# Performance work log

Measured on AMD Instinct MI355X. Metric: run time of the kernel, lower is better.

Reference implementation:

```python
import jax, jax.numpy as jnp
import numpy as np

N = 50000
E = 1600000
DIM = 128
RC = 5.0
DEPTH = 3


def setup_inputs() -> dict:
    key = jax.random.key(0)
    kv, ke, ks, kd, kw, kb, krs, ksig = jax.random.split(key, 8)
    v = jax.random.normal(kv, (N, DIM), dtype=jnp.float32)
    # edge distances in [0, rc]
    e = jax.random.uniform(ke, (E, 1), dtype=jnp.float32) * RC
    src = jax.random.randint(ks, (E,), 0, N, dtype=jnp.int32)
    dst = jax.random.randint(kd, (E,), 0, N, dtype=jnp.int32)
    # learned params: A = nn.Linear(dim, dim); rs, sigma = torch.rand(1)
    A_w = jax.random.normal(kw, (DIM, DIM), dtype=jnp.float32) / np.sqrt(DIM)
    A_b = jax.random.normal(kb, (DIM,), dtype=jnp.float32) * 0.01
    rs = jax.random.uniform(krs, (1,), dtype=jnp.float32)
    sigma = jax.random.uniform(ksig, (1,), dtype=jnp.float32)
    return {"v": v, "e": e, "src": src, "dst": dst,
            "A_w": A_w, "A_b": A_b, "rs": rs, "sigma": sigma}


def _edge_envelope(r, rs, sigma):
    # exp(-(r-rs)^2/sigma^2) * 0.5 * cos(pi*r/rc) * (r < rc)
    gauss = jnp.exp(-jnp.square(r - rs) / jnp.square(sigma))
    cutoff = 0.5 * jnp.cos(np.pi * r / RC) * (r < RC).astype(r.dtype)
    return gauss * cutoff


def reference(v, e, src, dst, A_w, A_b, rs, sigma):
    f = _edge_envelope(e, rs, sigma)  # [E, 1]
    cur = v
    for _ in range(DEPTH):
        msg = f * cur[src]  # gather src node feats, weight by edge envelope: [E, DIM]
        svf = jax.ops.segment_sum(msg, dst, num_segments=N)  # scatter-sum to dst: [N, DIM]
        cur = jax.nn.relu((svf + v) @ A_w.T + A_b)  # linear + relu, skip from original v
    return cur
```

## Files before the change

### kernel.cpp

```cpp
#include <hip/hip_runtime.h>
#include <math.h>

#define N_NODES 50000
#define N_PAD   50048
#define N_EDGES 1600000
#define DIM     128
#define RCUT    5.0f
#define NGROUP  (N_PAD / 64)
#define NB_PRE  512
#define CH_PRE  (N_EDGES / NB_PRE)
#define NB_CONV 6250
#define NB_WPREP 8
#define NB_SUB  8
#define B_SUB   (NB_PRE / NB_SUB)
#define XPAD    136

typedef __attribute__((ext_vector_type(8))) __bf16 bf16x8;
typedef __attribute__((ext_vector_type(4))) float  f32x4;

__device__ __forceinline__ float bf_lo(unsigned int u) { return __uint_as_float(u << 16); }
__device__ __forceinline__ float bf_hi(unsigned int u) { return __uint_as_float(u & 0xffff0000u); }
__device__ __forceinline__ unsigned short f2bf(float x) {
    unsigned int u = __float_as_uint(x);
    u += 0x7fffu + ((u >> 16) & 1u);
    return (unsigned short)(u >> 16);
}

__global__ __launch_bounds__(256) void preA_kernel(
        const float* __restrict__ v, unsigned short* __restrict__ vb,
        const float* __restrict__ Aw, uint4* __restrict__ wfrag,
        const int* __restrict__ dst, int* __restrict__ partial) {
    int b = blockIdx.x;
    if (b < NB_CONV) {
        int i = b * 256 + threadIdx.x;
        float4 x = ((const float4*)v)[i];
        uint2 o;
        o.x = (unsigned)f2bf(x.x) | ((unsigned)f2bf(x.y) << 16);
        o.y = (unsigned)f2bf(x.z) | ((unsigned)f2bf(x.w) << 16);
        ((uint2*)vb)[i] = o;
    } else if (b < NB_CONV + NB_WPREP) {
        int t = (b - NB_CONV) * 256 + threadIdx.x;
        int lane = t & 63, nt = (t >> 6) & 7, kk = t >> 9;
        int n  = nt * 16 + (lane & 15);
        int k0 = kk * 32 + (lane >> 4) * 8;
        unsigned short h[8];
        #pragma unroll
        for (int i = 0; i < 8; ++i) h[i] = f2bf(Aw[n * DIM + k0 + i]);
        uint4 o;
        o.x = h[0] | ((unsigned)h[1] << 16); o.y = h[2] | ((unsigned)h[3] << 16);
        o.z = h[4] | ((unsigned)h[5] << 16); o.w = h[6] | ((unsigned)h[7] << 16);
        wfrag[t] = o;
    } else {
        __shared__ int h[NGROUP];
        int cb = b - NB_CONV - NB_WPREP, tid = threadIdx.x;
        for (int g = tid; g < NGROUP; g += 256) h[g] = 0;
        __syncthreads();
        int beg = cb * CH_PRE, end = beg + CH_PRE;
        for (int i = beg + tid; i < end; i += 256)
            atomicAdd(&h[dst[i] >> 6], 1);
        __syncthreads();
        for (int g = tid; g < NGROUP; g += 256) partial[cb * NGROUP + g] = h[g];
    }
}

__global__ __launch_bounds__(256) void ktot2_kernel(const int* __restrict__ partial,
                                                    int* __restrict__ partial2) {
    int gb = blockIdx.x & 3, bb = blockIdx.x >> 2;
    int g = gb * 256 + threadIdx.x;
    if (g >= NGROUP) return;
    int s = 0;
    int b0 = bb * B_SUB;
    for (int b = b0; b < b0 + B_SUB; ++b) s += partial[b * NGROUP + g];
    partial2[bb * NGROUP + g] = s;
}

__global__ __launch_bounds__(256) void kscan_kernel(const int* __restrict__ partial2,
                                                    int* __restrict__ goff) {
    __shared__ int part[256];
    int tid = threadIdx.x;
    int i0 = tid * 4;
    int v[4]; int s = 0;
    #pragma unroll
    for (int k = 0; k < 4; ++k) {
        int i = i0 + k; int t = 0;
        if (i < NGROUP) {
            #pragma unroll
            for (int bb = 0; bb < NB_SUB; ++bb) t += partial2[bb * NGROUP + i];
        }
        v[k] = t; s += t;
    }
    part[tid] = s; __syncthreads();
    for (int d = 1; d < 256; d <<= 1) {
        int val = (tid >= d) ? part[tid - d] : 0;
        __syncthreads(); part[tid] += val; __syncthreads();
    }
    int run = (tid == 0) ? 0 : part[tid - 1];
    #pragma unroll
    for (int k = 0; k < 4; ++k) {
        int i = i0 + k;
        if (i < NGROUP) { goff[i] = run; run += v[k]; }
    }
    if (tid == 0) goff[NGROUP] = N_EDGES;
}

__global__ __launch_bounds__(256) void kbase2_kernel(const int* __restrict__ partial,
                                                     const int* __restrict__ partial2,
                                                     const int* __restrict__ goff,
                                                     int* __restrict__ pbase) {
    int gb = blockIdx.x & 3, bb = blockIdx.x >> 2;
    int g = gb * 256 + threadIdx.x;
    if (g >= NGROUP) return;
    int run = goff[g];
    for (int b2 = 0; b2 < bb; ++b2) run += partial2[b2 * NGROUP + g];
    int b0 = bb * B_SUB;
    for (int b = b0; b < b0 + B_SUB; ++b) {
        pbase[b * NGROUP + g] = run;
        run += partial[b * NGROUP + g];
    }
}

__global__ __launch_bounds__(512) void reorder_kernel(
        const float* __restrict__ e,
        const int*   __restrict__ src,
        const int*   __restrict__ dst,
        const float* __restrict__ rs,
        const float* __restrict__ sigma,
        const int*   __restrict__ pbase,
        int2* __restrict__ metaT) {
    __shared__ int base[NGROUP];
    __shared__ int cnt[NGROUP];
    int b = blockIdx.x, tid = threadIdx.x;
    for (int g = tid; g < NGROUP; g += 512) { base[g] = pbase[b * NGROUP + g]; cnt[g] = 0; }
    __syncthreads();
    float rsv = rs[0], sg = sigma[0];
    int beg = b * CH_PRE, end = beg + CH_PRE;
    for (int i = beg + tid; i < end; i += 512) {
        float r  = e[i];
        float d  = r - rsv;
        float gauss = expf(-(d * d) / (sg * sg));
        float cut   = 0.5f * cosf(r * (float)(M_PI / (double)RCUT));
        cut = (r < RCUT) ? cut : 0.0f;
        float fe = gauss * cut;
        int dn = dst[i];
        int g  = dn >> 6;
        int lr = atomicAdd(&cnt[g], 1);
        metaT[base[g] + lr] = make_int2(src[i] * (DIM * 2) | ((dn & 63) << 24),
                                        __float_as_int(fe));
    }
}

__global__ __launch_bounds__(256) void tagsort_kernel(
        const int2* __restrict__ metaT,
        const int*  __restrict__ goff,
        int2* __restrict__ meta,
        int*  __restrict__ off) {
    __shared__ int cnt[64], base[64], cur[64];
    int g = blockIdx.x, tid = threadIdx.x;
    int sbeg = goff[g], send = goff[g + 1];
    if (tid < 64) cnt[tid] = 0;
    __syncthreads();
    for (int i = sbeg + tid; i < send; i += 256)
        atomicAdd(&cnt[(metaT[i].x >> 24) & 63], 1);
    __syncthreads();
    if (tid == 0) {
        int run = 0;
        #pragma unroll
        for (int t = 0; t < 64; ++t) { base[t] = run; cur[t] = run; run += cnt[t]; }
    }
    __syncthreads();
    if (tid < 64) {
        int node = g * 64 + tid;
        if (node <= N_NODES) off[node] = sbeg + base[tid];
    }
    __syncthreads();
    for (int i = sbeg + tid; i < send; i += 256) {
        int2 m = metaT[i];
        int tag = (m.x >> 24) & 63;
        int lr = atomicAdd(&cur[tag], 1);
        meta[sbeg + lr] = make_int2(m.x & 0x00FFFFFF, m.y);
    }
}

#define EDGE2(mx, mf, rr)                                        \
    do {                                                         \
        float ff = __int_as_float(mf);                           \
        a0 = fmaf(ff, bf_lo(rr), a0);                            \
        a1 = fmaf(ff, bf_hi(rr), a1);                            \
    } while (0)

__global__ __launch_bounds__(512, 6) void layer_kernel(
        const unsigned short* __restrict__ cur,
        const unsigned short* __restrict__ vb,
        const int2*  __restrict__ meta,
        const int*   __restrict__ off,
        const uint4* __restrict__ wfrag,
        const float* __restrict__ bias,
        unsigned short* __restrict__ out_bf,
        float* __restrict__ out_f,
        int last) {
    __shared__ unsigned short xlds[64 * XPAD];
    int tid  = threadIdx.x;
    int wv   = tid >> 6, lane = tid & 63;
    int g    = blockIdx.x;
    int n0   = g * 64 + wv * 8;

    int offidx = n0 + ((lane < 9) ? lane : 8);
    if (offidx > N_NODES) offidx = N_NODES;
    int myoff = off[offidx];

    const char* basec = (const char*)cur + lane * 4;

    #pragma unroll 1
    for (int q = 0; q < 8; ++q) {
        int nl = wv * 8 + q;
        int n  = n0 + q;
        float a0 = 0.f, a1 = 0.f;
        if (n < N_NODES) {
            unsigned vv = *(const unsigned*)((const char*)vb + (size_t)n * (DIM * 2) + lane * 4);
            a0 = bf_lo(vv); a1 = bf_hi(vv);
            int beg = __builtin_amdgcn_readlane(myoff, q);
            int end = __builtin_amdgcn_readlane(myoff, q + 1);
            int c = beg;
            if ((c & 1) && c < end) {
                int2 m = meta[c];
                unsigned rr = *(const unsigned*)(basec + (unsigned)m.x);
                EDGE2(m.x, m.y, rr);
                ++c;
            }
            for (; c + 16 <= end; c += 16) {
                int4 m0 = *(const int4*)(meta + c);
                int4 m1 = *(const int4*)(meta + c + 2);
                int4 m2 = *(const int4*)(meta + c + 4);
                int4 m3 = *(const int4*)(meta + c + 6);
                int4 m4 = *(const int4*)(meta + c + 8);
                int4 m5 = *(const int4*)(meta + c + 10);
                int4 m6 = *(const int4*)(meta + c + 12);
                int4 m7 = *(const int4*)(meta + c + 14);
                unsigned r0  = *(const unsigned*)(basec + (unsigned)m0.x);
                unsigned r1  = *(const unsigned*)(basec + (unsigned)m0.z);
                unsigned r2  = *(const unsigned*)(basec + (unsigned)m1.x);
                unsigned r3  = *(const unsigned*)(basec + (unsigned)m1.z);
                unsigned r4  = *(const unsigned*)(basec + (unsigned)m2.x);
                unsigned r5  = *(const unsigned*)(basec + (unsigned)m2.z);
                unsigned r6  = *(const unsigned*)(basec + (unsigned)m3.x);
                unsigned r7  = *(const unsigned*)(basec + (unsigned)m3.z);
                unsigned r8  = *(const unsigned*)(basec + (unsigned)m4.x);
                unsigned r9  = *(const unsigned*)(basec + (unsigned)m4.z);
                unsigned r10 = *(const unsigned*)(basec + (unsigned)m5.x);
                unsigned r11 = *(const unsigned*)(basec + (unsigned)m5.z);
                unsigned r12 = *(const unsigned*)(basec + (unsigned)m6.x);
                unsigned r13 = *(const unsigned*)(basec + (unsigned)m6.z);
                unsigned r14 = *(const unsigned*)(basec + (unsigned)m7.x);
                unsigned r15 = *(const unsigned*)(basec + (unsigned)m7.z);
                EDGE2(m0.x, m0.y, r0);  EDGE2(m0.z, m0.w, r1);
                EDGE2(m1.x, m1.y, r2);  EDGE2(m1.z, m1.w, r3);
                EDGE2(m2.x, m2.y, r4);  EDGE2(m2.z, m2.w, r5);
                EDGE2(m3.x, m3.y, r6);  EDGE2(m3.z, m3.w, r7);
                EDGE2(m4.x, m4.y, r8);  EDGE2(m4.z, m4.w, r9);
                EDGE2(m5.x, m5.y, r10); EDGE2(m5.z, m5.w, r11);
                EDGE2(m6.x, m6.y, r12); EDGE2(m6.z, m6.w, r13);
                EDGE2(m7.x, m7.y, r14); EDGE2(m7.z, m7.w, r15);
            }
            if (c + 8 <= end) {
                int4 m0 = *(const int4*)(meta + c);
                int4 m1 = *(const int4*)(meta + c + 2);
                int4 m2 = *(const int4*)(meta + c + 4);
                int4 m3 = *(const int4*)(meta + c + 6);
                unsigned r0 = *(const unsigned*)(basec + (unsigned)m0.x);
                unsigned r1 = *(const unsigned*)(basec + (unsigned)m0.z);
                unsigned r2 = *(const unsigned*)(basec + (unsigned)m1.x);
                unsigned r3 = *(const unsigned*)(basec + (unsigned)m1.z);
                unsigned r4 = *(const unsigned*)(basec + (unsigned)m2.x);
                unsigned r5 = *(const unsigned*)(basec + (unsigned)m2.z);
                unsigned r6 = *(const unsigned*)(basec + (unsigned)m3.x);
                unsigned r7 = *(const unsigned*)(basec + (unsigned)m3.z);
                EDGE2(m0.x, m0.y, r0); EDGE2(m0.z, m0.w, r1);
                EDGE2(m1.x, m1.y, r2); EDGE2(m1.z, m1.w, r3);
                EDGE2(m2.x, m2.y, r4); EDGE2(m2.z, m2.w, r5);
                EDGE2(m3.x, m3.y, r6); EDGE2(m3.z, m3.w, r7);
                c += 8;
            }
            for (; c < end; ++c) {
                int2 m = meta[c];
                unsigned rr = *(const unsigned*)(basec + (unsigned)m.x);
                EDGE2(m.x, m.y, rr);
            }
        }
        *(unsigned*)(xlds + nl * XPAD + lane * 2) =
            (unsigned)f2bf(a0) | ((unsigned)f2bf(a1) << 16);
    }
    __syncthreads();

    int quad = lane >> 4, l16 = lane & 15;
    int rb = wv >> 1, nh = wv & 1;
    f32x4 acc[4];
    #pragma unroll
    for (int j = 0; j < 4; ++j) acc[j] = (f32x4){0.f, 0.f, 0.f, 0.f};

    const unsigned short* xp = xlds + (rb * 16 + l16) * XPAD + quad * 8;
    #pragma unroll
    for (int kk = 0; kk < 4; ++kk) {
        bf16x8 af = *(const bf16x8*)(xp + kk * 32);
        #pragma unroll
        for (int j = 0; j < 4; ++j) {
            uint4 w = wfrag[(kk * 8 + nh * 4 + j) * 64 + lane];
            bf16x8 bfr = __builtin_bit_cast(bf16x8, w);
            acc[j] = __builtin_amdgcn_mfma_f32_16x16x32_bf16(af, bfr, acc[j], 0, 0, 0);
        }
    }

    int orow0 = g * 64 + rb * 16 + quad * 4;
    #pragma unroll
    for (int j = 0; j < 4; ++j) {
        int col = (nh * 4 + j) * 16 + l16;
        float b = bias[col];
        #pragma unroll
        for (int r = 0; r < 4; ++r) {
            int orow = orow0 + r;
            if (orow < N_NODES) {
                float val = fmaxf(acc[j][r] + b, 0.f);
                if (last) out_f[(size_t)orow * DIM + col] = val;
                else      out_bf[(size_t)orow * DIM + col] = f2bf(val);
            }
        }
    }
}

extern "C" void kernel_launch(void* const* d_in, const int* in_sizes, int n_in,
                              void* d_out, int out_size, void* d_ws, size_t ws_size,
                              hipStream_t stream) {
    const float* v     = (const float*)d_in[0];
    const float* e     = (const float*)d_in[1];
    const int*   src   = (const int*)  d_in[2];
    const int*   dst   = (const int*)  d_in[3];
    const float* Aw    = (const float*)d_in[4];
    const float* Ab    = (const float*)d_in[5];
    const float* rs    = (const float*)d_in[6];
    const float* sigma = (const float*)d_in[7];
    float* out = (float*)d_out;

    char* p = (char*)d_ws;
    int2*           meta  = (int2*)p;            p += (size_t)N_EDGES * 8;
    unsigned short* bufV  = (unsigned short*)p;  p += (size_t)N_PAD * DIM * 2;
    unsigned short* bufA  = (unsigned short*)p;  p += (size_t)N_PAD * DIM * 2;
    unsigned short* bufB  = (unsigned short*)p;  p += (size_t)N_PAD * DIM * 2;
    uint4*          wfrag = (uint4*)p;           p += 2048 * 16;
    int*            off   = (int*)p;             p += (size_t)(N_NODES + 1) * 4;
    int*            goff  = (int*)p;             p += (NGROUP + 2) * 4;
    int2* metaT    = (int2*)bufA;
    int*  partial  = (int*)bufB;
    int*  pbase    = partial + NB_PRE * NGROUP;
    int*  partial2 = pbase + NB_PRE * NGROUP;

    preA_kernel<<<NB_CONV + NB_WPREP + NB_PRE, 256, 0, stream>>>(
        v, bufV, Aw, wfrag, dst, partial);
    ktot2_kernel<<<4 * NB_SUB, 256, 0, stream>>>(partial, partial2);
    kscan_kernel<<<1, 256, 0, stream>>>(partial2, goff);
    kbase2_kernel<<<4 * NB_SUB, 256, 0, stream>>>(partial, partial2, goff, pbase);
    reorder_kernel<<<NB_PRE, 512, 0, stream>>>(e, src, dst, rs, sigma, pbase, metaT);
    tagsort_kernel<<<NGROUP, 256, 0, stream>>>(metaT, goff, meta, off);

    layer_kernel<<<NGROUP, 512, 0, stream>>>(bufV, bufV, meta, off, wfrag, Ab, bufB, nullptr, 0);
    layer_kernel<<<NGROUP, 512, 0, stream>>>(bufB, bufV, meta, off, wfrag, Ab, bufA, nullptr, 0);
    layer_kernel<<<NGROUP, 512, 0, stream>>>(bufA, bufV, meta, off, wfrag, Ab, nullptr, out, 1);
}
```

Measured before the change: 345.3 us.

## Fuse all preprocessing and layer kernels into one persistent kernel with grid barriers

Replaces the nine separate launches (histogram, scans, reorder, tagsort, three layers) with a single persistent mega-kernel. It sizes the grid from occupancy and uses atomic-counter grid barriers between phases. The goal is to remove per-launch overhead and tail idle time between small kernels. The risks are lower parallelism in the layer phases, the cost of spinning at each barrier, a possible deadlock if not all blocks are co-resident, and a hardcoded count of 256 CUs.

```diff
diff --git a/kernel.cpp b/kernel.cpp
--- a/kernel.cpp
+++ b/kernel.cpp
@@ -7,13 +7,9 @@
 #define DIM     128
 #define RCUT    5.0f
 #define NGROUP  (N_PAD / 64)
-#define NB_PRE  512
-#define CH_PRE  (N_EDGES / NB_PRE)
-#define NB_CONV 6250
-#define NB_WPREP 8
-#define NB_SUB  8
-#define B_SUB   (NB_PRE / NB_SUB)
+#define NSUB    16
 #define XPAD    136
+#define MAXNB   1024
 
 typedef __attribute__((ext_vector_type(8))) __bf16 bf16x8;
 typedef __attribute__((ext_vector_type(4))) float  f32x4;
@@ -26,159 +22,16 @@
     return (unsigned short)(u >> 16);
 }
 
-__global__ __launch_bounds__(256) void preA_kernel(
-        const float* __restrict__ v, unsigned short* __restrict__ vb,
-        const float* __restrict__ Aw, uint4* __restrict__ wfrag,
-        const int* __restrict__ dst, int* __restrict__ partial) {
-    int b = blockIdx.x;
-    if (b < NB_CONV) {
-        int i = b * 256 + threadIdx.x;
-        float4 x = ((const float4*)v)[i];
-        uint2 o;
-        o.x = (unsigned)f2bf(x.x) | ((unsigned)f2bf(x.y) << 16);
-        o.y = (unsigned)f2bf(x.z) | ((unsigned)f2bf(x.w) << 16);
-        ((uint2*)vb)[i] = o;
-    } else if (b < NB_CONV + NB_WPREP) {
-        int t = (b - NB_CONV) * 256 + threadIdx.x;
-        int lane = t & 63, nt = (t >> 6) & 7, kk = t >> 9;
-        int n  = nt * 16 + (lane & 15);
-        int k0 = kk * 32 + (lane >> 4) * 8;
-        unsigned short h[8];
-        #pragma unroll
-        for (int i = 0; i < 8; ++i) h[i] = f2bf(Aw[n * DIM + k0 + i]);
-        uint4 o;
-        o.x = h[0] | ((unsigned)h[1] << 16); o.y = h[2] | ((unsigned)h[3] << 16);
-        o.z = h[4] | ((unsigned)h[5] << 16); o.w = h[6] | ((unsigned)h[7] << 16);
-        wfrag[t] = o;
-    } else {
-        __shared__ int h[NGROUP];
-        int cb = b - NB_CONV - NB_WPREP, tid = threadIdx.x;
-        for (int g = tid; g < NGROUP; g += 256) h[g] = 0;
-        __syncthreads();
-        int beg = cb * CH_PRE, end = beg + CH_PRE;
-        for (int i = beg + tid; i < end; i += 256)
-            atomicAdd(&h[dst[i] >> 6], 1);
-        __syncthreads();
-        for (int g = tid; g < NGROUP; g += 256) partial[cb * NGROUP + g] = h[g];
-    }
-}
-
-__global__ __launch_bounds__(256) void ktot2_kernel(const int* __restrict__ partial,
-                                                    int* __restrict__ partial2) {
-    int gb = blockIdx.x & 3, bb = blockIdx.x >> 2;
-    int g = gb * 256 + threadIdx.x;
-    if (g >= NGROUP) return;
-    int s = 0;
-    int b0 = bb * B_SUB;
-    for (int b = b0; b < b0 + B_SUB; ++b) s += partial[b * NGROUP + g];
-    partial2[bb * NGROUP + g] = s;
-}
-
-__global__ __launch_bounds__(256) void kscan_kernel(const int* __restrict__ partial2,
-                                                    int* __restrict__ goff) {
-    __shared__ int part[256];
-    int tid = threadIdx.x;
-    int i0 = tid * 4;
-    int v[4]; int s = 0;
-    #pragma unroll
-    for (int k = 0; k < 4; ++k) {
-        int i = i0 + k; int t = 0;
-        if (i < NGROUP) {
-            #pragma unroll
-            for (int bb = 0; bb < NB_SUB; ++bb) t += partial2[bb * NGROUP + i];
-        }
-        v[k] = t; s += t;
-    }
-    part[tid] = s; __syncthreads();
-    for (int d = 1; d < 256; d <<= 1) {
-        int val = (tid >= d) ? part[tid - d] : 0;
-        __syncthreads(); part[tid] += val; __syncthreads();
-    }
-    int run = (tid == 0) ? 0 : part[tid - 1];
-    #pragma unroll
-    for (int k = 0; k < 4; ++k) {
-        int i = i0 + k;
-        if (i < NGROUP) { goff[i] = run; run += v[k]; }
-    }
-    if (tid == 0) goff[NGROUP] = N_EDGES;
-}
-
-__global__ __launch_bounds__(256) void kbase2_kernel(const int* __restrict__ partial,
-                                                     const int* __restrict__ partial2,
-                                                     const int* __restrict__ goff,
-                                                     int* __restrict__ pbase) {
-    int gb = blockIdx.x & 3, bb = blockIdx.x >> 2;
-    int g = gb * 256 + threadIdx.x;
-    if (g >= NGROUP) return;
-    int run = goff[g];
-    for (int b2 = 0; b2 < bb; ++b2) run += partial2[b2 * NGROUP + g];
-    int b0 = bb * B_SUB;
-    for (int b = b0; b < b0 + B_SUB; ++b) {
-        pbase[b * NGROUP + g] = run;
-        run += partial[b * NGROUP + g];
-    }
-}
-
-__global__ __launch_bounds__(512) void reorder_kernel(
-        const float* __restrict__ e,
-        const int*   __restrict__ src,
-        const int*   __restrict__ dst,
-        const float* __restrict__ rs,
-        const float* __restrict__ sigma,
-        const int*   __restrict__ pbase,
-        int2* __restrict__ metaT) {
-    __shared__ int base[NGROUP];
-    __shared__ int cnt[NGROUP];
-    int b = blockIdx.x, tid = threadIdx.x;
-    for (int g = tid; g < NGROUP; g += 512) { base[g] = pbase[b * NGROUP + g]; cnt[g] = 0; }
+__device__ __forceinline__ void gsync(int* bar, int idx, int nb) {
     __syncthreads();
-    float rsv = rs[0], sg = sigma[0];
-    int beg = b * CH_PRE, end = beg + CH_PRE;
-    for (int i = beg + tid; i < end; i += 512) {
-        float r  = e[i];
-        float d  = r - rsv;
-        float gauss = expf(-(d * d) / (sg * sg));
-        float cut   = 0.5f * cosf(r * (float)(M_PI / (double)RCUT));
-        cut = (r < RCUT) ? cut : 0.0f;
-        float fe = gauss * cut;
-        int dn = dst[i];
-        int g  = dn >> 6;
-        int lr = atomicAdd(&cnt[g], 1);
-        metaT[base[g] + lr] = make_int2(src[i] * (DIM * 2) | ((dn & 63) << 24),
-                                        __float_as_int(fe));
-    }
-}
-
-__global__ __launch_bounds__(256) void tagsort_kernel(
-        const int2* __restrict__ metaT,
-        const int*  __restrict__ goff,
-        int2* __restrict__ meta,
-        int*  __restrict__ off) {
-    __shared__ int cnt[64], base[64], cur[64];
-    int g = blockIdx.x, tid = threadIdx.x;
-    int sbeg = goff[g], send = goff[g + 1];
-    if (tid < 64) cnt[tid] = 0;
+    if (threadIdx.x == 0) {
+        __threadfence();
+        __hip_atomic_fetch_add(&bar[idx], 1, __ATOMIC_RELAXED, __HIP_MEMORY_SCOPE_AGENT);
+        while (__hip_atomic_load(&bar[idx], __ATOMIC_RELAXED, __HIP_MEMORY_SCOPE_AGENT) < nb)
+            __builtin_amdgcn_s_sleep(2);
+        __threadfence();
+    }
     __syncthreads();
-    for (int i = sbeg + tid; i < send; i += 256)
-        atomicAdd(&cnt[(metaT[i].x >> 24) & 63], 1);
-    __syncthreads();
-    if (tid == 0) {
-        int run = 0;
-        #pragma unroll
-        for (int t = 0; t < 64; ++t) { base[t] = run; cur[t] = run; run += cnt[t]; }
-    }
-    __syncthreads();
-    if (tid < 64) {
-        int node = g * 64 + tid;
-        if (node <= N_NODES) off[node] = sbeg + base[tid];
-    }
-    __syncthreads();
-    for (int i = sbeg + tid; i < send; i += 256) {
-        int2 m = metaT[i];
-        int tag = (m.x >> 24) & 63;
-        int lr = atomicAdd(&cur[tag], 1);
-        meta[sbeg + lr] = make_int2(m.x & 0x00FFFFFF, m.y);
-    }
 }
 
 #define EDGE2(mx, mf, rr)                                        \
@@ -188,7 +41,7 @@
         a1 = fmaf(ff, bf_hi(rr), a1);                            \
     } while (0)
 
-__global__ __launch_bounds__(512, 6) void layer_kernel(
+__device__ __forceinline__ void layer_body(
         const unsigned short* __restrict__ cur,
         const unsigned short* __restrict__ vb,
         const int2*  __restrict__ meta,
@@ -197,11 +50,9 @@
         const float* __restrict__ bias,
         unsigned short* __restrict__ out_bf,
         float* __restrict__ out_f,
-        int last) {
-    __shared__ unsigned short xlds[64 * XPAD];
+        int last, int g, unsigned short* xlds) {
     int tid  = threadIdx.x;
     int wv   = tid >> 6, lane = tid & 63;
-    int g    = blockIdx.x;
     int n0   = g * 64 + wv * 8;
 
     int offidx = n0 + ((lane < 9) ? lane : 8);
@@ -326,6 +177,174 @@
     }
 }
 
+__global__ __launch_bounds__(512, 8) void mega_kernel(
+        const float* __restrict__ v, const float* __restrict__ e,
+        const int* __restrict__ src, const int* __restrict__ dst,
+        const float* __restrict__ Aw, const float* __restrict__ Ab,
+        const float* __restrict__ rs, const float* __restrict__ sigma,
+        float* __restrict__ out,
+        int2* __restrict__ meta, unsigned short* __restrict__ bufV,
+        unsigned short* __restrict__ bufA, unsigned short* __restrict__ bufB,
+        uint4* __restrict__ wfrag, int* __restrict__ off, int* __restrict__ goff,
+        int* __restrict__ partial, int* __restrict__ partial2,
+        int* __restrict__ pbase, int* __restrict__ bar) {
+    __shared__ __align__(16) char smem[64 * XPAD * 2];
+    const int bid = blockIdx.x, tid = threadIdx.x;
+    const int NB = gridDim.x, GT = NB * 512;
+    const int gid = bid * 512 + tid;
+    const int CH  = (N_EDGES + NB - 1) / NB;
+    const int ebeg = bid * CH;
+    const int eend = (ebeg + CH < N_EDGES) ? ebeg + CH : N_EDGES;
+
+    for (int i = gid; i < N_NODES * DIM / 4; i += GT) {
+        float4 x = ((const float4*)v)[i];
+        uint2 o;
+        o.x = (unsigned)f2bf(x.x) | ((unsigned)f2bf(x.y) << 16);
+        o.y = (unsigned)f2bf(x.z) | ((unsigned)f2bf(x.w) << 16);
+        ((uint2*)bufV)[i] = o;
+    }
+    if (gid < 2048) {
+        int t = gid;
+        int lane = t & 63, nt = (t >> 6) & 7, kk = t >> 9;
+        int n  = nt * 16 + (lane & 15);
+        int k0 = kk * 32 + (lane >> 4) * 8;
+        unsigned short h[8];
+        #pragma unroll
+        for (int i = 0; i < 8; ++i) h[i] = f2bf(Aw[n * DIM + k0 + i]);
+        uint4 o;
+        o.x = h[0] | ((unsigned)h[1] << 16); o.y = h[2] | ((unsigned)h[3] << 16);
+        o.z = h[4] | ((unsigned)h[5] << 16); o.w = h[6] | ((unsigned)h[7] << 16);
+        wfrag[t] = o;
+    }
+    {
+        int* h = (int*)smem;
+        for (int g = tid; g < NGROUP; g += 512) h[g] = 0;
+        __syncthreads();
+        for (int i = ebeg + tid; i < eend; i += 512)
+            atomicAdd(&h[dst[i] >> 6], 1);
+        __syncthreads();
+        for (int g = tid; g < NGROUP; g += 512) partial[bid * NGROUP + g] = h[g];
+    }
+    gsync(bar, 0, NB);
+
+    const int BS = (NB + NSUB - 1) / NSUB;
+    for (int id = gid; id < NSUB * NGROUP; id += GT) {
+        int bb = id / NGROUP, g = id - bb * NGROUP;
+        int b0 = bb * BS, b1 = (b0 + BS < NB) ? b0 + BS : NB;
+        int s = 0;
+        for (int b = b0; b < b1; ++b) s += partial[b * NGROUP + g];
+        partial2[bb * NGROUP + g] = s;
+    }
+    gsync(bar, 1, NB);
+
+    if (bid == 0) {
+        int* part = (int*)smem;
+        int i0 = tid * 2;
+        int vv[2]; int s = 0;
+        #pragma unroll
+        for (int k = 0; k < 2; ++k) {
+            int i = i0 + k; int t = 0;
+            if (i < NGROUP) {
+                #pragma unroll
+                for (int bb = 0; bb < NSUB; ++bb) t += partial2[bb * NGROUP + i];
+            }
+            vv[k] = t; s += t;
+        }
+        part[tid] = s; __syncthreads();
+        for (int d = 1; d < 512; d <<= 1) {
+            int val = (tid >= d) ? part[tid - d] : 0;
+            __syncthreads(); part[tid] += val; __syncthreads();
+        }
+        int run = (tid == 0) ? 0 : part[tid - 1];
+        #pragma unroll
+        for (int k = 0; k < 2; ++k) {
+            int i = i0 + k;
+            if (i < NGROUP) { goff[i] = run; run += vv[k]; }
+        }
+        if (tid == 0) goff[NGROUP] = N_EDGES;
+    }
+    gsync(bar, 2, NB);
+
+    for (int id = gid; id < NSUB * NGROUP; id += GT) {
+        int bb = id / NGROUP, g = id - bb * NGROUP;
+        int run = goff[g];
+        for (int b2 = 0; b2 < bb; ++b2) run += partial2[b2 * NGROUP + g];
+        int b0 = bb * BS, b1 = (b0 + BS < NB) ? b0 + BS : NB;
+        for (int b = b0; b < b1; ++b) {
+            pbase[b * NGROUP + g] = run;
+            run += partial[b * NGROUP + g];
+        }
+    }
+    gsync(bar, 3, NB);
+
+    {
+        int* base = (int*)smem;
+        int* cnt  = base + NGROUP;
+        for (int g = tid; g < NGROUP; g += 512) {
+            base[g] = pbase[bid * NGROUP + g]; cnt[g] = 0;
+        }
+        __syncthreads();
+        float rsv = rs[0], sg = sigma[0];
+        int2* metaT = (int2*)bufA;
+        for (int i = ebeg + tid; i < eend; i += 512) {
+            float r  = e[i];
+            float d  = r - rsv;
+            float gauss = expf(-(d * d) / (sg * sg));
+            float cut   = 0.5f * cosf(r * (float)(M_PI / (double)RCUT));
+            cut = (r < RCUT) ? cut : 0.0f;
+            float fe = gauss * cut;
+            int dn = dst[i];
+            int g  = dn >> 6;
+            int lr = atomicAdd(&cnt[g], 1);
+            metaT[base[g] + lr] = make_int2(src[i] * (DIM * 2) | ((dn & 63) << 24),
+                                            __float_as_int(fe));
+        }
+    }
+    gsync(bar, 4, NB);
+
+    for (int g = bid; g < NGROUP; g += NB) {
+        __syncthreads();
+        int* c64 = (int*)smem; int* b64 = c64 + 64; int* cu64 = b64 + 64;
+        const int2* metaT = (const int2*)bufA;
+        int sbeg = goff[g], send = goff[g + 1];
+        if (tid < 64) c64[tid] = 0;
+        __syncthreads();
+        for (int i = sbeg + tid; i < send; i += 512)
+            atomicAdd(&c64[(metaT[i].x >> 24) & 63], 1);
+        __syncthreads();
+        if (tid == 0) {
+            int run = 0;
+            #pragma unroll
+            for (int t = 0; t < 64; ++t) { b64[t] = run; cu64[t] = run; run += c64[t]; }
+        }
+        __syncthreads();
+        if (tid < 64) {
+            int node = g * 64 + tid;
+            if (node <= N_NODES) off[node] = sbeg + b64[tid];
+        }
+        __syncthreads();
+        for (int i = sbeg + tid; i < send; i += 512) {
+            int2 m = metaT[i];
+            int tag = (m.x >> 24) & 63;
+            int lr = atomicAdd(&cu64[tag], 1);
+            meta[sbeg + lr] = make_int2(m.x & 0x00FFFFFF, m.y);
+        }
+    }
+    gsync(bar, 5, NB);
+
+    unsigned short* xlds = (unsigned short*)smem;
+    for (int L = 0; L < 3; ++L) {
+        const unsigned short* curp = (L == 0) ? bufV : ((L == 1) ? bufB : bufA);
+        unsigned short* outb = (L == 0) ? bufB : bufA;
+        for (int g = bid; g < NGROUP; g += NB) {
+            __syncthreads();
+            layer_body(curp, bufV, meta, off, wfrag, Ab,
+                       outb, out, (L == 2) ? 1 : 0, g, xlds);
+        }
+        if (L < 2) gsync(bar, 6 + L, NB);
+    }
+}
+
 extern "C" void kernel_launch(void* const* d_in, const int* in_sizes, int n_in,
                               void* d_out, int out_size, void* d_ws, size_t ws_size,
                               hipStream_t stream) {
@@ -347,20 +366,23 @@
     uint4*          wfrag = (uint4*)p;           p += 2048 * 16;
     int*            off   = (int*)p;             p += (size_t)(N_NODES + 1) * 4;
     int*            goff  = (int*)p;             p += (NGROUP + 2) * 4;
-    int2* metaT    = (int2*)bufA;
-    int*  partial  = (int*)bufB;
-    int*  pbase    = partial + NB_PRE * NGROUP;
-    int*  partial2 = pbase + NB_PRE * NGROUP;
-
-    preA_kernel<<<NB_CONV + NB_WPREP + NB_PRE, 256, 0, stream>>>(
-        v, bufV, Aw, wfrag, dst, partial);
-    ktot2_kernel<<<4 * NB_SUB, 256, 0, stream>>>(partial, partial2);
-    kscan_kernel<<<1, 256, 0, stream>>>(partial2, goff);
-    kbase2_kernel<<<4 * NB_SUB, 256, 0, stream>>>(partial, partial2, goff, pbase);
-    reorder_kernel<<<NB_PRE, 512, 0, stream>>>(e, src, dst, rs, sigma, pbase, metaT);
-    tagsort_kernel<<<NGROUP, 256, 0, stream>>>(metaT, goff, meta, off);
-
-    layer_kernel<<<NGROUP, 512, 0, stream>>>(bufV, bufV, meta, off, wfrag, Ab, bufB, nullptr, 0);
-    layer_kernel<<<NGROUP, 512, 0, stream>>>(bufB, bufV, meta, off, wfrag, Ab, bufA, nullptr, 0);
-    layer_kernel<<<NGROUP, 512, 0, stream>>>(bufA, bufV, meta, off, wfrag, Ab, nullptr, out, 1);
-}
+    int*            bar   = (int*)p;             p += 16 * 4;
+    int* partial  = (int*)bufB;
+    int* partial2 = partial + MAXNB * NGROUP;
+    int* pbase    = partial2 + NSUB * NGROUP;
+
+    static int maxblk = 0;
+    if (maxblk == 0) {
+        if (hipOccupancyMaxActiveBlocksPerMultiprocessor(&maxblk, mega_kernel, 512, 0)
+                != hipSuccess || maxblk <= 0)
+            maxblk = 2;
+    }
+    int nb = maxblk * 256;
+    if (nb > NGROUP) nb = NGROUP;
+
+    hipMemsetAsync(bar, 0, 16 * 4, stream);
+    mega_kernel<<<nb, 512, 0, stream>>>(
+        v, e, src, dst, Aw, Ab, rs, sigma, out,
+        meta, bufV, bufA, bufB, wfrag, off, goff,
+        partial, partial2, pbase, bar);
+}
```

Result: slower. 908.1 us (+163.0%).

## Fuse tag sort into first layer kernel and use smaller 16-node blocks for later layers

Applied to the files above, without the earlier changes.

Removes the separate tagsort kernel and performs the per-group local sort inside the first layer kernel. The sorted meta is written out for later layers and the gather reads it back right after, so it should stay in cache. Layers 1 and 2 now use 128-thread blocks covering 16 nodes each instead of 512-thread blocks covering 64 nodes. The smaller blocks are meant to balance the irregular gather load and raise occupancy. The cost is that each block reloads the weight fragments and does a smaller MFMA tile, and layer 0 gains extra sort work before its gather.

```diff
diff --git a/kernel.cpp b/kernel.cpp
--- a/kernel.cpp
+++ b/kernel.cpp
@@ -14,6 +14,7 @@
 #define NB_SUB  8
 #define B_SUB   (NB_PRE / NB_SUB)
 #define XPAD    136
+#define NTILE   (N_PAD / 16)
 
 typedef __attribute__((ext_vector_type(8))) __bf16 bf16x8;
 typedef __attribute__((ext_vector_type(4))) float  f32x4;
@@ -149,38 +150,6 @@
     }
 }
 
-__global__ __launch_bounds__(256) void tagsort_kernel(
-        const int2* __restrict__ metaT,
-        const int*  __restrict__ goff,
-        int2* __restrict__ meta,
-        int*  __restrict__ off) {
-    __shared__ int cnt[64], base[64], cur[64];
-    int g = blockIdx.x, tid = threadIdx.x;
-    int sbeg = goff[g], send = goff[g + 1];
-    if (tid < 64) cnt[tid] = 0;
-    __syncthreads();
-    for (int i = sbeg + tid; i < send; i += 256)
-        atomicAdd(&cnt[(metaT[i].x >> 24) & 63], 1);
-    __syncthreads();
-    if (tid == 0) {
-        int run = 0;
-        #pragma unroll
-        for (int t = 0; t < 64; ++t) { base[t] = run; cur[t] = run; run += cnt[t]; }
-    }
-    __syncthreads();
-    if (tid < 64) {
-        int node = g * 64 + tid;
-        if (node <= N_NODES) off[node] = sbeg + base[tid];
-    }
-    __syncthreads();
-    for (int i = sbeg + tid; i < send; i += 256) {
-        int2 m = metaT[i];
-        int tag = (m.x >> 24) & 63;
-        int lr = atomicAdd(&cur[tag], 1);
-        meta[sbeg + lr] = make_int2(m.x & 0x00FFFFFF, m.y);
-    }
-}
-
 #define EDGE2(mx, mf, rr)                                        \
     do {                                                         \
         float ff = __int_as_float(mf);                           \
@@ -188,26 +157,120 @@
         a1 = fmaf(ff, bf_hi(rr), a1);                            \
     } while (0)
 
-__global__ __launch_bounds__(512, 6) void layer_kernel(
+__device__ __forceinline__ void gather_node(
+        const int2* __restrict__ meta, const char* basec,
+        int beg, int end, float& a0, float& a1) {
+    int c = beg;
+    if ((c & 1) && c < end) {
+        int2 m = meta[c];
+        unsigned rr = *(const unsigned*)(basec + (unsigned)m.x);
+        EDGE2(m.x, m.y, rr);
+        ++c;
+    }
+    for (; c + 16 <= end; c += 16) {
+        int4 m0 = *(const int4*)(meta + c);
+        int4 m1 = *(const int4*)(meta + c + 2);
+        int4 m2 = *(const int4*)(meta + c + 4);
+        int4 m3 = *(const int4*)(meta + c + 6);
+        int4 m4 = *(const int4*)(meta + c + 8);
+        int4 m5 = *(const int4*)(meta + c + 10);
+        int4 m6 = *(const int4*)(meta + c + 12);
+        int4 m7 = *(const int4*)(meta + c + 14);
+        unsigned r0  = *(const unsigned*)(basec + (unsigned)m0.x);
+        unsigned r1  = *(const unsigned*)(basec + (unsigned)m0.z);
+        unsigned r2  = *(const unsigned*)(basec + (unsigned)m1.x);
+        unsigned r3  = *(const unsigned*)(basec + (unsigned)m1.z);
+        unsigned r4  = *(const unsigned*)(basec + (unsigned)m2.x);
+        unsigned r5  = *(const unsigned*)(basec + (unsigned)m2.z);
+        unsigned r6  = *(const unsigned*)(basec + (unsigned)m3.x);
+        unsigned r7  = *(const unsigned*)(basec + (unsigned)m3.z);
+        unsigned r8  = *(const unsigned*)(basec + (unsigned)m4.x);
+        unsigned r9  = *(const unsigned*)(basec + (unsigned)m4.z);
+        unsigned r10 = *(const unsigned*)(basec + (unsigned)m5.x);
+        unsigned r11 = *(const unsigned*)(basec + (unsigned)m5.z);
+        unsigned r12 = *(const unsigned*)(basec + (unsigned)m6.x);
+        unsigned r13 = *(const unsigned*)(basec + (unsigned)m6.z);
+        unsigned r14 = *(const unsigned*)(basec + (unsigned)m7.x);
+        unsigned r15 = *(const unsigned*)(basec + (unsigned)m7.z);
+        EDGE2(m0.x, m0.y, r0);  EDGE2(m0.z, m0.w, r1);
+        EDGE2(m1.x, m1.y, r2);  EDGE2(m1.z, m1.w, r3);
+        EDGE2(m2.x, m2.y, r4);  EDGE2(m2.z, m2.w, r5);
+        EDGE2(m3.x, m3.y, r6);  EDGE2(m3.z, m3.w, r7);
+        EDGE2(m4.x, m4.y, r8);  EDGE2(m4.z, m4.w, r9);
+        EDGE2(m5.x, m5.y, r10); EDGE2(m5.z, m5.w, r11);
+        EDGE2(m6.x, m6.y, r12); EDGE2(m6.z, m6.w, r13);
+        EDGE2(m7.x, m7.y, r14); EDGE2(m7.z, m7.w, r15);
+    }
+    if (c + 8 <= end) {
+        int4 m0 = *(const int4*)(meta + c);
+        int4 m1 = *(const int4*)(meta + c + 2);
+        int4 m2 = *(const int4*)(meta + c + 4);
+        int4 m3 = *(const int4*)(meta + c + 6);
+        unsigned r0 = *(const unsigned*)(basec + (unsigned)m0.x);
+        unsigned r1 = *(const unsigned*)(basec + (unsigned)m0.z);
+        unsigned r2 = *(const unsigned*)(basec + (unsigned)m1.x);
+        unsigned r3 = *(const unsigned*)(basec + (unsigned)m1.z);
+        unsigned r4 = *(const unsigned*)(basec + (unsigned)m2.x);
+        unsigned r5 = *(const unsigned*)(basec + (unsigned)m2.z);
+        unsigned r6 = *(const unsigned*)(basec + (unsigned)m3.x);
+        unsigned r7 = *(const unsigned*)(basec + (unsigned)m3.z);
+        EDGE2(m0.x, m0.y, r0); EDGE2(m0.z, m0.w, r1);
+        EDGE2(m1.x, m1.y, r2); EDGE2(m1.z, m1.w, r3);
+        EDGE2(m2.x, m2.y, r4); EDGE2(m2.z, m2.w, r5);
+        EDGE2(m3.x, m3.y, r6); EDGE2(m3.z, m3.w, r7);
+        c += 8;
+    }
+    for (; c < end; ++c) {
+        int2 m = meta[c];
+        unsigned rr = *(const unsigned*)(basec + (unsigned)m.x);
+        EDGE2(m.x, m.y, rr);
+    }
+}
+
+__global__ __launch_bounds__(512) void layer0_kernel(
         const unsigned short* __restrict__ cur,
         const unsigned short* __restrict__ vb,
-        const int2*  __restrict__ meta,
-        const int*   __restrict__ off,
+        const int2*  __restrict__ metaT,
+        const int*   __restrict__ goff,
+        int2* __restrict__ meta,
+        int*  __restrict__ off,
         const uint4* __restrict__ wfrag,
         const float* __restrict__ bias,
-        unsigned short* __restrict__ out_bf,
-        float* __restrict__ out_f,
-        int last) {
+        unsigned short* __restrict__ out_bf) {
     __shared__ unsigned short xlds[64 * XPAD];
-    int tid  = threadIdx.x;
-    int wv   = tid >> 6, lane = tid & 63;
-    int g    = blockIdx.x;
-    int n0   = g * 64 + wv * 8;
-
-    int offidx = n0 + ((lane < 9) ? lane : 8);
-    if (offidx > N_NODES) offidx = N_NODES;
-    int myoff = off[offidx];
-
+    __shared__ int c64[64], b64[65], cu64[64];
+    int tid = threadIdx.x;
+    int wv  = tid >> 6, lane = tid & 63;
+    int g   = blockIdx.x;
+    int sbeg = goff[g], send = goff[g + 1];
+
+    if (tid < 64) c64[tid] = 0;
+    __syncthreads();
+    for (int i = sbeg + tid; i < send; i += 512)
+        atomicAdd(&c64[(metaT[i].x >> 24) & 63], 1);
+    __syncthreads();
+    if (tid == 0) {
+        int run = 0;
+        #pragma unroll
+        for (int t = 0; t < 64; ++t) { b64[t] = run; cu64[t] = run; run += c64[t]; }
+        b64[64] = run;
+    }
+    __syncthreads();
+    if (tid < 64) {
+        int node = g * 64 + tid;
+        if (node <= N_NODES) off[node] = sbeg + b64[tid];
+    }
+    for (int i = sbeg + tid; i < send; i += 512) {
+        int2 m = metaT[i];
+        int tag = (m.x >> 24) & 63;
+        int lr = atomicAdd(&cu64[tag], 1);
+        meta[sbeg + lr] = make_int2(m.x & 0x00FFFFFF, m.y);
+    }
+    __syncthreads();
+
+    int n0 = g * 64 + wv * 8;
+    int myoff = 0;
+    if (lane < 9) myoff = sbeg + b64[wv * 8 + lane];
     const char* basec = (const char*)cur + lane * 4;
 
     #pragma unroll 1
@@ -220,71 +283,7 @@
             a0 = bf_lo(vv); a1 = bf_hi(vv);
             int beg = __builtin_amdgcn_readlane(myoff, q);
             int end = __builtin_amdgcn_readlane(myoff, q + 1);
-            int c = beg;
-            if ((c & 1) && c < end) {
-                int2 m = meta[c];
-                unsigned rr = *(const unsigned*)(basec + (unsigned)m.x);
-                EDGE2(m.x, m.y, rr);
-                ++c;
-            }
-            for (; c + 16 <= end; c += 16) {
-                int4 m0 = *(const int4*)(meta + c);
-                int4 m1 = *(const int4*)(meta + c + 2);
-                int4 m2 = *(const int4*)(meta + c + 4);
-                int4 m3 = *(const int4*)(meta + c + 6);
-                int4 m4 = *(const int4*)(meta + c + 8);
-                int4 m5 = *(const int4*)(meta + c + 10);
-                int4 m6 = *(const int4*)(meta + c + 12);
-                int4 m7 = *(const int4*)(meta + c + 14);
-                unsigned r0  = *(const unsigned*)(basec + (unsigned)m0.x);
-                unsigned r1  = *(const unsigned*)(basec + (unsigned)m0.z);
-                unsigned r2  = *(const unsigned*)(basec + (unsigned)m1.x);
-                unsigned r3  = *(const unsigned*)(basec + (unsigned)m1.z);
-                unsigned r4  = *(const unsigned*)(basec + (unsigned)m2.x);
-                unsigned r5  = *(const unsigned*)(basec + (unsigned)m2.z);
-                unsigned r6  = *(const unsigned*)(basec + (unsigned)m3.x);
-                unsigned r7  = *(const unsigned*)(basec + (unsigned)m3.z);
-                unsigned r8  = *(const unsigned*)(basec + (unsigned)m4.x);
-                unsigned r9  = *(const unsigned*)(basec + (unsigned)m4.z);
-                unsigned r10 = *(const unsigned*)(basec + (unsigned)m5.x);
-                unsigned r11 = *(const unsigned*)(basec + (unsigned)m5.z);
-                unsigned r12 = *(const unsigned*)(basec + (unsigned)m6.x);
-                unsigned r13 = *(const unsigned*)(basec + (unsigned)m6.z);
-                unsigned r14 = *(const unsigned*)(basec + (unsigned)m7.x);
-                unsigned r15 = *(const unsigned*)(basec + (unsigned)m7.z);
-                EDGE2(m0.x, m0.y, r0);  EDGE2(m0.z, m0.w, r1);
-                EDGE2(m1.x, m1.y, r2);  EDGE2(m1.z, m1.w, r3);
-                EDGE2(m2.x, m2.y, r4);  EDGE2(m2.z, m2.w, r5);
-                EDGE2(m3.x, m3.y, r6);  EDGE2(m3.z, m3.w, r7);
-                EDGE2(m4.x, m4.y, r8);  EDGE2(m4.z, m4.w, r9);
-                EDGE2(m5.x, m5.y, r10); EDGE2(m5.z, m5.w, r11);
-                EDGE2(m6.x, m6.y, r12); EDGE2(m6.z, m6.w, r13);
-                EDGE2(m7.x, m7.y, r14); EDGE2(m7.z, m7.w, r15);
-            }
-            if (c + 8 <= end) {
-                int4 m0 = *(const int4*)(meta + c);
-                int4 m1 = *(const int4*)(meta + c + 2);
-                int4 m2 = *(const int4*)(meta + c + 4);
-                int4 m3 = *(const int4*)(meta + c + 6);
-                unsigned r0 = *(const unsigned*)(basec + (unsigned)m0.x);
-                unsigned r1 = *(const unsigned*)(basec + (unsigned)m0.z);
-                unsigned r2 = *(const unsigned*)(basec + (unsigned)m1.x);
-                unsigned r3 = *(const unsigned*)(basec + (unsigned)m1.z);
-                unsigned r4 = *(const unsigned*)(basec + (unsigned)m2.x);
-                unsigned r5 = *(const unsigned*)(basec + (unsigned)m2.z);
-                unsigned r6 = *(const unsigned*)(basec + (unsigned)m3.x);
-                unsigned r7 = *(const unsigned*)(basec + (unsigned)m3.z);
-                EDGE2(m0.x, m0.y, r0); EDGE2(m0.z, m0.w, r1);
-                EDGE2(m1.x, m1.y, r2); EDGE2(m1.z, m1.w, r3);
-                EDGE2(m2.x, m2.y, r4); EDGE2(m2.z, m2.w, r5);
-                EDGE2(m3.x, m3.y, r6); EDGE2(m3.z, m3.w, r7);
-                c += 8;
-            }
-            for (; c < end; ++c) {
-                int2 m = meta[c];
-                unsigned rr = *(const unsigned*)(basec + (unsigned)m.x);
-                EDGE2(m.x, m.y, rr);
-            }
+            gather_node(meta, basec, beg, end, a0, a1);
         }
         *(unsigned*)(xlds + nl * XPAD + lane * 2) =
             (unsigned)f2bf(a0) | ((unsigned)f2bf(a1) << 16);
@@ -313,6 +312,75 @@
     #pragma unroll
     for (int j = 0; j < 4; ++j) {
         int col = (nh * 4 + j) * 16 + l16;
+        float b = bias[col];
+        #pragma unroll
+        for (int r = 0; r < 4; ++r) {
+            int orow = orow0 + r;
+            if (orow < N_NODES)
+                out_bf[(size_t)orow * DIM + col] = f2bf(fmaxf(acc[j][r] + b, 0.f));
+        }
+    }
+}
+
+__global__ __launch_bounds__(128, 8) void layer12_kernel(
+        const unsigned short* __restrict__ cur,
+        const unsigned short* __restrict__ vb,
+        const int2*  __restrict__ meta,
+        const int*   __restrict__ off,
+        const uint4* __restrict__ wfrag,
+        const float* __restrict__ bias,
+        unsigned short* __restrict__ out_bf,
+        float* __restrict__ out_f,
+        int last) {
+    __shared__ unsigned short xlds[16 * XPAD];
+    int tid = threadIdx.x;
+    int wv  = tid >> 6, lane = tid & 63;
+    int tile = blockIdx.x;
+    int n0  = tile * 16 + wv * 8;
+
+    int offidx = n0 + ((lane < 9) ? lane : 8);
+    if (offidx > N_NODES) offidx = N_NODES;
+    int myoff = off[offidx];
+    const char* basec = (const char*)cur + lane * 4;
+
+    #pragma unroll 1
+    for (int q = 0; q < 8; ++q) {
+        int nl = wv * 8 + q;
+        int n  = n0 + q;
+        float a0 = 0.f, a1 = 0.f;
+        if (n < N_NODES) {
+            unsigned vv = *(const unsigned*)((const char*)vb + (size_t)n * (DIM * 2) + lane * 4);
+            a0 = bf_lo(vv); a1 = bf_hi(vv);
+            int beg = __builtin_amdgcn_readlane(myoff, q);
+            int end = __builtin_amdgcn_readlane(myoff, q + 1);
+            gather_node(meta, basec, beg, end, a0, a1);
+        }
+        *(unsigned*)(xlds + nl * XPAD + lane * 2) =
+            (unsigned)f2bf(a0) | ((unsigned)f2bf(a1) << 16);
+    }
+    __syncthreads();
+
+    int quad = lane >> 4, l16 = lane & 15;
+    f32x4 acc[4];
+    #pragma unroll
+    for (int j = 0; j < 4; ++j) acc[j] = (f32x4){0.f, 0.f, 0.f, 0.f};
+
+    const unsigned short* xp = xlds + l16 * XPAD + quad * 8;
+    #pragma unroll
+    for (int kk = 0; kk < 4; ++kk) {
+        bf16x8 af = *(const bf16x8*)(xp + kk * 32);
+        #pragma unroll
+        for (int j = 0; j < 4; ++j) {
+            uint4 w = wfrag[(kk * 8 + wv * 4 + j) * 64 + lane];
+            bf16x8 bfr = __builtin_bit_cast(bf16x8, w);
+            acc[j] = __builtin_amdgcn_mfma_f32_16x16x32_bf16(af, bfr, acc[j], 0, 0, 0);
+        }
+    }
+
+    int orow0 = tile * 16 + quad * 4;
+    #pragma unroll
+    for (int j = 0; j < 4; ++j) {
+        int col = (wv * 4 + j) * 16 + l16;
         float b = bias[col];
         #pragma unroll
         for (int r = 0; r < 4; ++r) {
@@ -358,9 +426,11 @@
     kscan_kernel<<<1, 256, 0, stream>>>(partial2, goff);
     kbase2_kernel<<<4 * NB_SUB, 256, 0, stream>>>(partial, partial2, goff, pbase);
     reorder_kernel<<<NB_PRE, 512, 0, stream>>>(e, src, dst, rs, sigma, pbase, metaT);
-    tagsort_kernel<<<NGROUP, 256, 0, stream>>>(metaT, goff, meta, off);
-
-    layer_kernel<<<NGROUP, 512, 0, stream>>>(bufV, bufV, meta, off, wfrag, Ab, bufB, nullptr, 0);
-    layer_kernel<<<NGROUP, 512, 0, stream>>>(bufB, bufV, meta, off, wfrag, Ab, bufA, nullptr, 0);
-    layer_kernel<<<NGROUP, 512, 0, stream>>>(bufA, bufV, meta, off, wfrag, Ab, nullptr, out, 1);
-}
+
+    layer0_kernel<<<NGROUP, 512, 0, stream>>>(
+        bufV, bufV, metaT, goff, meta, off, wfrag, Ab, bufB);
+    layer12_kernel<<<NTILE, 128, 0, stream>>>(
+        bufB, bufV, meta, off, wfrag, Ab, bufA, nullptr, 0);
+    layer12_kernel<<<NTILE, 128, 0, stream>>>(
+        bufA, bufV, meta, off, wfrag, Ab, nullptr, out, 1);
+}
```

New measurement: 332.7 us. 1.04x faster.
